# Kernel tuning notes

Hardware: AMD Instinct MI355X
Metric: run time of the kernel (lower is better)

## Reference

```python
import jax, jax.numpy as jnp
import numpy as np

B, C, H, W = 8, 128, 256, 256
N_POS, N_NEG = 2048, 8192
TEMPERATURE = 1.0
EPS = 1e-6


def setup_inputs() -> dict:
    key = jax.random.key(0)
    k0, k1, k2, k3, k4, k5, k6 = jax.random.split(key, 7)
    predict_seg_map = jax.random.normal(k0, (B, C, H, W), dtype=jnp.float32)
    # Random pixel-location samples (stand-in for nonzero+randperm sampling,
    # which the original detaches -> constants w.r.t. the loss).
    pos_b = jax.random.randint(k1, (N_POS,), 0, B, dtype=jnp.int32)
    pos_h = jax.random.randint(k2, (N_POS,), 0, H, dtype=jnp.int32)
    pos_w = jax.random.randint(k3, (N_POS,), 0, W, dtype=jnp.int32)
    neg_b = jax.random.randint(k4, (N_NEG,), 0, B, dtype=jnp.int32)
    neg_h = jax.random.randint(k5, (N_NEG,), 0, H, dtype=jnp.int32)
    neg_w = jax.random.randint(k6, (N_NEG,), 0, W, dtype=jnp.int32)
    return {
        "predict_seg_map": predict_seg_map,
        "pos_b": pos_b, "pos_h": pos_h, "pos_w": pos_w,
        "neg_b": neg_b, "neg_h": neg_h, "neg_w": neg_w,
    }


def _l2_normalize(x):
    # Matches nn.CosineSimilarity(dim=-1, eps=1e-6): clamp norm from below.
    n = jnp.sqrt(jnp.sum(x * x, axis=-1, keepdims=True))
    return x / jnp.maximum(n, EPS)


def reference(predict_seg_map, pos_b, pos_h, pos_w, neg_b, neg_h, neg_w):
    # Irregular gather of pixel embeddings: [N, C]
    pos_logits = predict_seg_map[pos_b, :, pos_h, pos_w]
    neg_logits = predict_seg_map[neg_b, :, neg_h, neg_w]

    pos_n = _l2_normalize(pos_logits)  # [N_POS, C]
    neg_n = _l2_normalize(neg_logits)  # [N_NEG, C]

    # Cosine similarity matrices via GEMM on unit vectors.
    pos_sim = jnp.einsum('ic,jc->ij', pos_n, pos_n)  # [N_POS, N_POS]
    neg_sim = jnp.einsum('ic,jc->ij', pos_n, neg_n)  # [N_POS, N_NEG]

    exp_pos = jnp.exp(pos_sim / TEMPERATURE)
    # Original subtracts exp(1.0) (diagonal self-similarity at T=1).
    pos_row_sum = jnp.sum(exp_pos, axis=1) - jnp.exp(jnp.float32(1.0))
    neg_row_sum = jnp.sum(jnp.exp(neg_sim / TEMPERATURE), axis=1)

    likelihood = pos_row_sum / (pos_row_sum + neg_row_sum)
    nll = -jnp.mean(jnp.log(likelihood))
    return nll
```

## Files before the change

### kernel.cpp

```cpp
#include <hip/hip_runtime.h>
#include <hip/hip_bf16.h>
#include <math.h>

#define BB      8
#define C_CH    128
#define HH      256
#define WW      256
#define N_POS   2048
#define N_NEG   8192
#define N_ROWS  (N_POS + N_NEG)
#define EPS_N   1e-6f

#define NIG     (N_POS / 256)
#define NJS     (N_ROWS / 64)
#define NJSLAB      (N_ROWS / 64)
#define NJSLAB_POS  (N_POS / 64)

#define PANEL   512

typedef __attribute__((ext_vector_type(8))) short bf16x8;
typedef __attribute__((ext_vector_type(4))) float f32x4;


__global__ __launch_bounds__(256) void gather_norm_kernel(
    const float* __restrict__ seg,
    const int* __restrict__ pb, const int* __restrict__ ph, const int* __restrict__ pw,
    const int* __restrict__ nb, const int* __restrict__ nh, const int* __restrict__ nw,
    ushort* __restrict__ hi_t, ushort* __restrict__ lo_t)
{
    const int wave = threadIdx.x >> 6;
    const int lane = threadIdx.x & 63;
    const int row  = blockIdx.x * 4 + wave;
    if (row >= N_ROWS) return;

    int b, h, w;
    if (row < N_POS) { b = pb[row]; h = ph[row]; w = pw[row]; }
    else { const int r = row - N_POS; b = nb[r]; h = nh[r]; w = nw[r]; }

    const size_t cs   = (size_t)HH * WW;
    const size_t base = (size_t)b * C_CH * cs + (size_t)h * WW + (size_t)w;

    const float v0 = seg[base + (size_t)lane * cs];
    const float v1 = seg[base + (size_t)(lane + 64) * cs];

    float ss = v0 * v0 + v1 * v1;
#pragma unroll
    for (int m = 1; m < 64; m <<= 1) ss += __shfl_xor(ss, m, 64);

    const float n  = fmaxf(sqrtf(ss), EPS_N);
    const float u0 = v0 / n;
    const float u1 = v1 / n;

    const __hip_bfloat16 h0 = __float2bfloat16(u0);
    const __hip_bfloat16 h1 = __float2bfloat16(u1);
    const __hip_bfloat16 l0 = __float2bfloat16(u0 - __bfloat162float(h0));
    const __hip_bfloat16 l1 = __float2bfloat16(u1 - __bfloat162float(h1));

    const int tile = row >> 4;
    const int lr   = row & 15;

    const int e0 = lane;
    const int ks0 = e0 >> 5, lk0 = (e0 & 31) >> 3, ke0 = e0 & 7;
    const size_t o0 = ((size_t)(tile * 4 + ks0) * 64 + lk0 * 16 + lr) * 8 + ke0;

    const int e1 = lane + 64;
    const int ks1 = e1 >> 5, lk1 = (e1 & 31) >> 3, ke1 = e1 & 7;
    const size_t o1 = ((size_t)(tile * 4 + ks1) * 64 + lk1 * 16 + lr) * 8 + ke1;

    hi_t[o0] = __hip_bfloat16_raw(h0).x;  lo_t[o0] = __hip_bfloat16_raw(l0).x;
    hi_t[o1] = __hip_bfloat16_raw(h1).x;  lo_t[o1] = __hip_bfloat16_raw(l1).x;
}

__global__ __launch_bounds__(256) void sim_mfma_kernel(
    const ushort* __restrict__ hi_t, const ushort* __restrict__ lo_t,
    float* __restrict__ partial)
{
    __shared__ ushort ldsB[2][8192];

    const int bid = blockIdx.x;
    const int ig  = bid / NJS;
    const int js  = bid % NJS;
    const int t    = threadIdx.x;
    const int wv   = t >> 6;
    const int ln   = t & 63;

    {
        const size_t gb = (size_t)js * 8192;
#pragma unroll
        for (int c = 0; c < 4; ++c) {
            const int off = (c * 256 + t) * 8;
            *(bf16x8*)&ldsB[0][off] = *(const bf16x8*)&hi_t[gb + off];
            *(bf16x8*)&ldsB[1][off] = *(const bf16x8*)&lo_t[gb + off];
        }
    }
    __syncthreads();

    const int iw0 = ig * 256 + wv * 64;
    const int lr = ln & 15;
    const int lk = ln >> 4;

    f32x4 acc[4][4];
#pragma unroll
    for (int m = 0; m < 4; ++m)
#pragma unroll
        for (int n = 0; n < 4; ++n) acc[m][n] = (f32x4){0.f, 0.f, 0.f, 0.f};

#pragma unroll
    for (int ks = 0; ks < 4; ++ks) {
        bf16x8 ah[4], al[4], bh[4], bl[4];
#pragma unroll
        for (int m = 0; m < 4; ++m) {
            const size_t pa = ((size_t)((ig * 16 + wv * 4 + m) * 4 + ks)) * PANEL + ln * 8;
            ah[m] = *(const bf16x8*)&hi_t[pa];
            al[m] = *(const bf16x8*)&lo_t[pa];
        }
#pragma unroll
        for (int n = 0; n < 4; ++n) {
            const int lo_off = (n * 4 + ks) * PANEL + ln * 8;
            bh[n] = *(const bf16x8*)&ldsB[0][lo_off];
            bl[n] = *(const bf16x8*)&ldsB[1][lo_off];
        }

#pragma unroll
        for (int n = 0; n < 4; ++n) {
#pragma unroll
            for (int m = 0; m < 4; ++m) {
                acc[m][n] = __builtin_amdgcn_mfma_f32_16x16x32_bf16(ah[m], bh[n], acc[m][n], 0, 0, 0);
                acc[m][n] = __builtin_amdgcn_mfma_f32_16x16x32_bf16(ah[m], bl[n], acc[m][n], 0, 0, 0);
                acc[m][n] = __builtin_amdgcn_mfma_f32_16x16x32_bf16(al[m], bh[n], acc[m][n], 0, 0, 0);
            }
        }
    }

#pragma unroll
    for (int m = 0; m < 4; ++m) {
        float s0 = 0.f, s1 = 0.f, s2 = 0.f, s3 = 0.f;
#pragma unroll
        for (int n = 0; n < 4; ++n) {
            s0 += expf(acc[m][n][0]);
            s1 += expf(acc[m][n][1]);
            s2 += expf(acc[m][n][2]);
            s3 += expf(acc[m][n][3]);
        }
        float s[4] = {s0, s1, s2, s3};
#pragma unroll
        for (int r = 0; r < 4; ++r) {
            float v = s[r];
            v += __shfl_xor(v, 1, 64);
            v += __shfl_xor(v, 2, 64);
            v += __shfl_xor(v, 4, 64);
            v += __shfl_xor(v, 8, 64);
            if (lr == 0) {
                const int row = iw0 + m * 16 + lk * 4 + r;
                partial[(size_t)js * N_POS + row] = v;
            }
        }
    }
}

__global__ __launch_bounds__(256) void rowred_kernel(
    const float* __restrict__ partial, float* __restrict__ bsum)
{
    const int t   = threadIdx.x;
    const int row = blockIdx.x * 256 + t;

    float P = 0.f;
#pragma unroll
    for (int s = 0; s < NJSLAB_POS; ++s) P += partial[(size_t)s * N_POS + row];

    float a0 = 0.f, a1 = 0.f, a2 = 0.f, a3 = 0.f;
    for (int s0 = NJSLAB_POS; s0 < NJSLAB; s0 += 16) {
        float v[16];
#pragma unroll
        for (int i = 0; i < 16; ++i)
            v[i] = partial[(size_t)(s0 + i) * N_POS + row];
#pragma unroll
        for (int i = 0; i < 16; i += 4) {
            a0 += v[i]; a1 += v[i + 1]; a2 += v[i + 2]; a3 += v[i + 3];
        }
    }
    const float Nv = (a0 + a1) + (a2 + a3);

    const float p = P - 2.71828182845904523536f;
    const float term = logf(p) - logf(p + Nv);

    __shared__ float red[256];
    red[t] = term;
    __syncthreads();
    for (int s = 128; s > 0; s >>= 1) {
        if (t < s) red[t] += red[t + s];
        __syncthreads();
    }
    if (t == 0) bsum[blockIdx.x] = red[0];
}

__global__ __launch_bounds__(64) void final_kernel(
    const float* __restrict__ bsum, float* __restrict__ out)
{
    if (threadIdx.x == 0) {
        float s = 0.f;
#pragma unroll
        for (int i = 0; i < N_POS / 256; ++i) s += bsum[i];
        out[0] = -s / (float)N_POS;
    }
}

extern "C" void kernel_launch(void* const* d_in, const int* in_sizes, int n_in,
                              void* d_out, int out_size, void* d_ws, size_t ws_size,
                              hipStream_t stream)
{
    const float* seg = (const float*)d_in[0];
    const int* pb = (const int*)d_in[1];
    const int* ph = (const int*)d_in[2];
    const int* pw = (const int*)d_in[3];
    const int* nb = (const int*)d_in[4];
    const int* nh = (const int*)d_in[5];
    const int* nw = (const int*)d_in[6];
    float* out = (float*)d_out;

    ushort* hi_t = (ushort*)d_ws;
    ushort* lo_t = hi_t + (size_t)N_ROWS * C_CH;
    float* partial = (float*)(lo_t + (size_t)N_ROWS * C_CH);
    float* bsum    = partial + (size_t)NJSLAB * N_POS;

    gather_norm_kernel<<<dim3((N_ROWS + 3) / 4), dim3(256), 0, stream>>>(
        seg, pb, ph, pw, nb, nh, nw, hi_t, lo_t);

    sim_mfma_kernel<<<dim3(NIG * NJS), dim3(256), 0, stream>>>(hi_t, lo_t, partial);

    rowred_kernel<<<dim3(N_POS / 256), dim3(256), 0, stream>>>(partial, bsum);
    final_kernel<<<dim3(1), dim3(64), 0, stream>>>(bsum, out);
}
```

Baseline: 63.27 us.

## Merge two column slabs per 512-thread block and load B fragments per n

The similarity kernel now launches 512-thread blocks that each cover two adjacent 64-column slabs. The LDS buffer doubles so both slabs are staged together, and the eight waves split as four row groups by two slabs. B fragments are now read from LDS inside the n loop instead of all at once, which lowers register pressure. Block count halves and the per-block staging cost is shared, but each A panel is still loaded by two waves, and the larger LDS footprint may limit occupancy.

```diff
diff --git a/kernel.cpp b/kernel.cpp
--- a/kernel.cpp
+++ b/kernel.cpp
@@ -12,6 +12,7 @@
 #define EPS_N   1e-6f
 
 #define NIG     (N_POS / 256)
+#define NJG     (N_ROWS / 128)
 #define NJS     (N_ROWS / 64)
 #define NJSLAB      (N_ROWS / 64)
 #define NJSLAB_POS  (N_POS / 64)
@@ -71,31 +72,37 @@
     hi_t[o1] = __hip_bfloat16_raw(h1).x;  lo_t[o1] = __hip_bfloat16_raw(l1).x;
 }
 
-__global__ __launch_bounds__(256) void sim_mfma_kernel(
+__global__ __launch_bounds__(512) void sim_mfma_kernel(
     const ushort* __restrict__ hi_t, const ushort* __restrict__ lo_t,
     float* __restrict__ partial)
 {
-    __shared__ ushort ldsB[2][8192];
+    __shared__ ushort ldsB[2][2][8192];
 
     const int bid = blockIdx.x;
-    const int ig  = bid / NJS;
-    const int js  = bid % NJS;
+    const int ig  = bid / NJG;
+    const int jsg = bid % NJG;
     const int t    = threadIdx.x;
     const int wv   = t >> 6;
     const int ln   = t & 63;
+    const int wy   = wv & 3;
+    const int wx   = wv >> 2;
 
     {
-        const size_t gb = (size_t)js * 8192;
-#pragma unroll
-        for (int c = 0; c < 4; ++c) {
-            const int off = (c * 256 + t) * 8;
-            *(bf16x8*)&ldsB[0][off] = *(const bf16x8*)&hi_t[gb + off];
-            *(bf16x8*)&ldsB[1][off] = *(const bf16x8*)&lo_t[gb + off];
+        const size_t gb0 = (size_t)(jsg * 2 + 0) * 8192;
+        const size_t gb1 = (size_t)(jsg * 2 + 1) * 8192;
+#pragma unroll
+        for (int c = 0; c < 2; ++c) {
+            const int off = (c * 512 + t) * 8;
+            *(bf16x8*)&ldsB[0][0][off] = *(const bf16x8*)&hi_t[gb0 + off];
+            *(bf16x8*)&ldsB[0][1][off] = *(const bf16x8*)&lo_t[gb0 + off];
+            *(bf16x8*)&ldsB[1][0][off] = *(const bf16x8*)&hi_t[gb1 + off];
+            *(bf16x8*)&ldsB[1][1][off] = *(const bf16x8*)&lo_t[gb1 + off];
         }
     }
     __syncthreads();
 
-    const int iw0 = ig * 256 + wv * 64;
+    const int js  = jsg * 2 + wx;
+    const int iw0 = ig * 256 + wy * 64;
     const int lr = ln & 15;
     const int lk = ln >> 4;
 
@@ -107,27 +114,23 @@
 
 #pragma unroll
     for (int ks = 0; ks < 4; ++ks) {
-        bf16x8 ah[4], al[4], bh[4], bl[4];
+        bf16x8 ah[4], al[4];
 #pragma unroll
         for (int m = 0; m < 4; ++m) {
-            const size_t pa = ((size_t)((ig * 16 + wv * 4 + m) * 4 + ks)) * PANEL + ln * 8;
+            const size_t pa = ((size_t)((ig * 16 + wy * 4 + m) * 4 + ks)) * PANEL + ln * 8;
             ah[m] = *(const bf16x8*)&hi_t[pa];
             al[m] = *(const bf16x8*)&lo_t[pa];
         }
 #pragma unroll
         for (int n = 0; n < 4; ++n) {
             const int lo_off = (n * 4 + ks) * PANEL + ln * 8;
-            bh[n] = *(const bf16x8*)&ldsB[0][lo_off];
-            bl[n] = *(const bf16x8*)&ldsB[1][lo_off];
-        }
-
-#pragma unroll
-        for (int n = 0; n < 4; ++n) {
+            const bf16x8 bh = *(const bf16x8*)&ldsB[wx][0][lo_off];
+            const bf16x8 bl = *(const bf16x8*)&ldsB[wx][1][lo_off];
 #pragma unroll
             for (int m = 0; m < 4; ++m) {
-                acc[m][n] = __builtin_amdgcn_mfma_f32_16x16x32_bf16(ah[m], bh[n], acc[m][n], 0, 0, 0);
-                acc[m][n] = __builtin_amdgcn_mfma_f32_16x16x32_bf16(ah[m], bl[n], acc[m][n], 0, 0, 0);
-                acc[m][n] = __builtin_amdgcn_mfma_f32_16x16x32_bf16(al[m], bh[n], acc[m][n], 0, 0, 0);
+                acc[m][n] = __builtin_amdgcn_mfma_f32_16x16x32_bf16(ah[m], bh, acc[m][n], 0, 0, 0);
+                acc[m][n] = __builtin_amdgcn_mfma_f32_16x16x32_bf16(ah[m], bl, acc[m][n], 0, 0, 0);
+                acc[m][n] = __builtin_amdgcn_mfma_f32_16x16x32_bf16(al[m], bh, acc[m][n], 0, 0, 0);
             }
         }
     }
@@ -226,7 +229,7 @@
     gather_norm_kernel<<<dim3((N_ROWS + 3) / 4), dim3(256), 0, stream>>>(
         seg, pb, ph, pw, nb, nh, nw, hi_t, lo_t);
 
-    sim_mfma_kernel<<<dim3(NIG * NJS), dim3(256), 0, stream>>>(hi_t, lo_t, partial);
+    sim_mfma_kernel<<<dim3(NIG * NJG), dim3(512), 0, stream>>>(hi_t, lo_t, partial);
 
     rowred_kernel<<<dim3(N_POS / 256), dim3(256), 0, stream>>>(partial, bsum);
     final_kernel<<<dim3(1), dim3(64), 0, stream>>>(bsum, out);
```

After: 70.58 us. 1.12x slower.
